# Kernel tuning notes

Hardware: AMD Instinct MI355X
Metric: run time of the kernel (lower is better)

## Reference

```python
import jax, jax.numpy as jnp
import numpy as np

E, H, V, B, T = 512, 512, 32000, 64, 20


def setup_inputs() -> dict:
    key = jax.random.key(0)
    ks = jax.random.split(key, 10)
    s = 0.05
    return {
        "features": jax.random.normal(ks[0], (B, E), jnp.float32),
        "captions": jax.random.randint(ks[1], (B, T), 0, V),
        "lenghts": jax.random.randint(ks[2], (B,), 1, T),
        "emb_table": jax.random.normal(ks[3], (V, E), jnp.float32) * s,
        "w_ih": jax.random.normal(ks[4], (4 * H, E), jnp.float32) * s,
        "w_hh": jax.random.normal(ks[5], (4 * H, H), jnp.float32) * s,
        "b_ih": jax.random.normal(ks[6], (4 * H,), jnp.float32) * s,
        "b_hh": jax.random.normal(ks[7], (4 * H,), jnp.float32) * s,
        "fc_w": jax.random.normal(ks[8], (V, H), jnp.float32) * s,
        "fc_b": jax.random.normal(ks[9], (V,), jnp.float32) * s,
    }


def _lstm(xs, w_ih, w_hh, b_ih, b_hh):
    # xs: [B, T+1, E] -> hidden states [B, T+1, H], PyTorch gate order i,f,g,o
    b, _, _ = xs.shape
    h0 = jnp.zeros((b, w_hh.shape[1]), xs.dtype)
    c0 = jnp.zeros_like(h0)
    bias = b_ih + b_hh

    def step(carry, x_t):
        h, c = carry
        gates = x_t @ w_ih.T + h @ w_hh.T + bias  # [B, 4H]
        i, f, g, o = jnp.split(gates, 4, axis=-1)
        i, f, o = jax.nn.sigmoid(i), jax.nn.sigmoid(f), jax.nn.sigmoid(o)
        g = jnp.tanh(g)
        c = f * c + i * g
        h = o * jnp.tanh(c)
        return (h, c), h

    _, hs = jax.lax.scan(step, (h0, c0), jnp.swapaxes(xs, 0, 1))  # hs: [T+1, B, H]
    return jnp.swapaxes(hs, 0, 1)


def reference(features, captions, lenghts, emb_table, w_ih, w_hh, b_ih, b_hh, fc_w, fc_b):
    embeddings = emb_table[captions]                       # [B, T, E]
    xs = jnp.concatenate([features[:, None, :], embeddings], axis=1)  # [B, T+1, E]
    hs = _lstm(xs, w_ih, w_hh, b_ih, b_hh)[:, 1:, :]       # [B, T, H]
    logits = hs @ fc_w.T + fc_b                            # [B, T, V]
    # original loops softmax over each 1-D vocab slice == softmax over last axis
    return jax.nn.softmax(logits, axis=-1)
```

## Files before the change

kernel.cpp:

```cpp
#include <hip/hip_runtime.h>
#include <cstdint>
#include <cstddef>

#define E_DIM 512
#define H_DIM 512
#define V_DIM 32000
#define B_DIM 64
#define T_DIM 20

typedef _Float16 f16;
typedef _Float16 f16x8 __attribute__((ext_vector_type(8)));
typedef _Float16 f16x4 __attribute__((ext_vector_type(4)));
typedef float    f32x4 __attribute__((ext_vector_type(4)));

__device__ __forceinline__ void async_lds16(void* lds, const void* g) {
  __builtin_amdgcn_global_load_lds(
      (const __attribute__((address_space(1))) uint32_t*)g,
      (__attribute__((address_space(3))) uint32_t*)lds, 16, 0, 0);
}

__device__ __forceinline__ float sigmoidf_(float x) {
  return 1.0f / (1.0f + expf(-x));
}

__global__ __launch_bounds__(128) void gather_x16_kernel(
    const float* __restrict__ features, const int* __restrict__ captions,
    const float* __restrict__ emb, f16* __restrict__ x16) {
  const int m = blockIdx.x;
  const int j = threadIdx.x;
  f16x4 r4 = {(f16)0.f, (f16)0.f, (f16)0.f, (f16)0.f};
  if (m < 1344) {
    const int b = m / 21;
    const int t = m % 21;
    const float* src = (t == 0)
        ? features + (size_t)b * E_DIM
        : emb + (size_t)captions[b * T_DIM + (t - 1)] * E_DIM;
    const float4 v = ((const float4*)src)[j];
    r4.x = (f16)v.x; r4.y = (f16)v.y; r4.z = (f16)v.z; r4.w = (f16)v.w;
  }
  ((f16x4*)(x16 + (size_t)m * 512))[j] = r4;
}

__global__ __launch_bounds__(256) void convert_w_kernel(
    const float* __restrict__ w, f16* __restrict__ w16) {
  const int i = blockIdx.x * 256 + threadIdx.x;
  const float4 v = ((const float4*)w)[i];
  f16x4 r;
  r.x = (f16)v.x; r.y = (f16)v.y; r.z = (f16)v.z; r.w = (f16)v.w;
  ((f16x4*)w16)[i] = r;
}

__global__ __launch_bounds__(256) void bias_sum_kernel(
    const float* __restrict__ a, const float* __restrict__ b,
    float* __restrict__ o) {
  const int i = blockIdx.x * 256 + threadIdx.x;
  if (i < 2048) o[i] = a[i] + b[i];
}

__global__ __launch_bounds__(256) void gemm16_kernel(
    const f16* __restrict__ A, const f16* __restrict__ Bw,
    const float* __restrict__ bias, float* __restrict__ C, int ldc) {
  __shared__ f16 As[128 * 64];
  __shared__ f16 Bs[128 * 64];
  const int tid = threadIdx.x;
  const int lane = tid & 63;
  const int wid = tid >> 6;
  const int m0 = blockIdx.y * 128;
  const int n0 = blockIdx.x * 128;
  const int wm = (wid >> 1) * 64;
  const int wn = (wid & 1) * 64;

  f32x4 acc[4][4];
#pragma unroll
  for (int i = 0; i < 4; ++i)
#pragma unroll
    for (int j = 0; j < 4; ++j) {
      f32x4 z = {0.f, 0.f, 0.f, 0.f};
      acc[i][j] = z;
    }
  const int lr = lane & 15;
  const int lkb = (lane >> 4) * 8;

  for (int kt = 0; kt < 512; kt += 64) {
#pragma unroll
    for (int i = 0; i < 4; ++i) {
      const int off = i * 4096 + wid * 1024 + lane * 16;
      const int row = off >> 7;
      const int colh = (off & 127) >> 1;
      async_lds16((char*)As + i * 4096 + wid * 1024,
                  A + (size_t)(m0 + row) * 512 + kt + colh);
      async_lds16((char*)Bs + i * 4096 + wid * 1024,
                  Bw + (size_t)(n0 + row) * 512 + kt + colh);
    }
    __syncthreads();
#pragma unroll
    for (int ks = 0; ks < 2; ++ks) {
      f16x8 af[4], bf[4];
#pragma unroll
      for (int mi = 0; mi < 4; ++mi)
        af[mi] = *(const f16x8*)&As[(wm + mi * 16 + lr) * 64 + ks * 32 + lkb];
#pragma unroll
      for (int ni = 0; ni < 4; ++ni)
        bf[ni] = *(const f16x8*)&Bs[(wn + ni * 16 + lr) * 64 + ks * 32 + lkb];
#pragma unroll
      for (int mi = 0; mi < 4; ++mi)
#pragma unroll
        for (int ni = 0; ni < 4; ++ni)
          acc[mi][ni] = __builtin_amdgcn_mfma_f32_16x16x32_f16(
              af[mi], bf[ni], acc[mi][ni], 0, 0, 0);
    }
    __syncthreads();
  }

#pragma unroll
  for (int mi = 0; mi < 4; ++mi) {
    const int mbase = m0 + wm + mi * 16 + (lane >> 4) * 4;
#pragma unroll
    for (int ni = 0; ni < 4; ++ni) {
      const int n = n0 + wn + ni * 16 + lr;
      const float bv = bias[n];
#pragma unroll
      for (int r = 0; r < 4; ++r)
        C[(size_t)(mbase + r) * ldc + n] = acc[mi][ni][r] + bv;
    }
  }
}

__global__ __launch_bounds__(256) void gemm16_f16out_kernel(
    const f16* __restrict__ A, const f16* __restrict__ Bw,
    const float* __restrict__ bias, f16* __restrict__ C16) {
  __shared__ f16 As[128 * 64];
  __shared__ f16 Bs[128 * 64];
  const int tid = threadIdx.x;
  const int lane = tid & 63;
  const int wid = tid >> 6;
  const int m0 = blockIdx.y * 128;
  const int n0 = blockIdx.x * 128;
  const int wm = (wid >> 1) * 64;
  const int wn = (wid & 1) * 64;

  f32x4 acc[4][4];
#pragma unroll
  for (int i = 0; i < 4; ++i)
#pragma unroll
    for (int j = 0; j < 4; ++j) {
      f32x4 z = {0.f, 0.f, 0.f, 0.f};
      acc[i][j] = z;
    }
  const int lr = lane & 15;
  const int lkb = (lane >> 4) * 8;

  for (int kt = 0; kt < 512; kt += 64) {
#pragma unroll
    for (int i = 0; i < 4; ++i) {
      const int off = i * 4096 + wid * 1024 + lane * 16;
      const int row = off >> 7;
      const int colh = (off & 127) >> 1;
      async_lds16((char*)As + i * 4096 + wid * 1024,
                  A + (size_t)(m0 + row) * 512 + kt + colh);
      async_lds16((char*)Bs + i * 4096 + wid * 1024,
                  Bw + (size_t)(n0 + row) * 512 + kt + colh);
    }
    __syncthreads();
#pragma unroll
    for (int ks = 0; ks < 2; ++ks) {
      f16x8 af[4], bf[4];
#pragma unroll
      for (int mi = 0; mi < 4; ++mi)
        af[mi] = *(const f16x8*)&As[(wm + mi * 16 + lr) * 64 + ks * 32 + lkb];
#pragma unroll
      for (int ni = 0; ni < 4; ++ni)
        bf[ni] = *(const f16x8*)&Bs[(wn + ni * 16 + lr) * 64 + ks * 32 + lkb];
#pragma unroll
      for (int mi = 0; mi < 4; ++mi)
#pragma unroll
        for (int ni = 0; ni < 4; ++ni)
          acc[mi][ni] = __builtin_amdgcn_mfma_f32_16x16x32_f16(
              af[mi], bf[ni], acc[mi][ni], 0, 0, 0);
    }
    __syncthreads();
  }

#pragma unroll
  for (int mi = 0; mi < 4; ++mi) {
    const int mbase = m0 + wm + mi * 16 + (lane >> 4) * 4;
#pragma unroll
    for (int ni = 0; ni < 4; ++ni) {
      const int n = n0 + wn + ni * 16 + lr;
      const float bv = bias[n];
#pragma unroll
      for (int r = 0; r < 4; ++r)
        C16[(size_t)(mbase + r) * 32000 + n] = (f16)(acc[mi][ni][r] + bv);
    }
  }
}

__global__ __launch_bounds__(256) void lstm_step_direct(
    const float* __restrict__ P, const f16* __restrict__ Whh,
    const f16* __restrict__ h_in, f16* __restrict__ h_out,
    float* __restrict__ c, f16* __restrict__ hs16, int t) {
  const int tid = threadIdx.x;
  const int lane = tid & 63;
  const int w = tid >> 6;
  const int u0 = blockIdx.x * 4;
  const int fr = lane & 15;
  const int fq = lane >> 4;
  const int grow = (fr >> 2) * 512 + u0 + (fr & 3);

  f32x4 acc = {0.f, 0.f, 0.f, 0.f};
  if (t > 0) {
    const f16* arow = h_in + (size_t)(w * 16 + fr) * 512;
    const f16* brow = Whh + (size_t)grow * 512;
    f16x8 a[16], b[16];
#pragma unroll
    for (int kk = 0; kk < 16; ++kk) {
      const int kc = kk * 32 + fq * 8;
      a[kk] = *(const f16x8*)&arow[kc];
      b[kk] = *(const f16x8*)&brow[kc];
    }
#pragma unroll
    for (int kk = 0; kk < 16; ++kk)
      acc = __builtin_amdgcn_mfma_f32_16x16x32_f16(a[kk], b[kk], acc, 0, 0, 0);
  }

#pragma unroll
  for (int r = 0; r < 4; ++r) {
    const int b = w * 16 + fq * 4 + r;
    acc[r] += P[((size_t)b * 21 + t) * 2048 + grow];
  }

#pragma unroll
  for (int r = 0; r < 4; ++r) {
    const float x  = acc[r];
    const float xf = __shfl_xor(x, 4);
    const float xg = __shfl_xor(x, 8);
    const float xo = __shfl_xor(x, 12);
    if (fr < 4) {
      const int b = w * 16 + fq * 4 + r;
      const int u = u0 + fr;
      const size_t bu = (size_t)b * 512 + u;
      const float si = sigmoidf_(x);
      const float sf = sigmoidf_(xf);
      const float tg = tanhf(xg);
      const float so = sigmoidf_(xo);
      const float cn = sf * c[bu] + si * tg;
      c[bu] = cn;
      const float hn = so * tanhf(cn);
      h_out[bu] = (f16)hn;
      if (t >= 1)
        hs16[((size_t)b * T_DIM + (t - 1)) * 512 + u] = (f16)hn;
    }
  }
}

__device__ __forceinline__ float waveMax(float v) {
#pragma unroll
  for (int o = 32; o > 0; o >>= 1) v = fmaxf(v, __shfl_down(v, o));
  return v;
}
__device__ __forceinline__ float waveSum(float v) {
#pragma unroll
  for (int o = 32; o > 0; o >>= 1) v += __shfl_down(v, o);
  return v;
}

__global__ __launch_bounds__(1024) void softmax_f16_kernel(
    const f16* __restrict__ lg, float* __restrict__ out) {
  const f16x8* L = (const f16x8*)(lg + (size_t)blockIdx.x * V_DIM);
  float4* p4 = (float4*)(out + (size_t)blockIdx.x * V_DIM);
  const int t = threadIdx.x;
  __shared__ float sred[16];

  float4 v[8];
  float m = -1e30f;
#pragma unroll
  for (int j = 0; j < 4; ++j) {
    const int i = j * 1024 + t;
    if (i < 4000) {
      const f16x8 h = L[i];
      v[2 * j].x     = (float)h[0]; v[2 * j].y     = (float)h[1];
      v[2 * j].z     = (float)h[2]; v[2 * j].w     = (float)h[3];
      v[2 * j + 1].x = (float)h[4]; v[2 * j + 1].y = (float)h[5];
      v[2 * j + 1].z = (float)h[6]; v[2 * j + 1].w = (float)h[7];
      m = fmaxf(m, fmaxf(fmaxf(v[2 * j].x, v[2 * j].y),
                         fmaxf(v[2 * j].z, v[2 * j].w)));
      m = fmaxf(m, fmaxf(fmaxf(v[2 * j + 1].x, v[2 * j + 1].y),
                         fmaxf(v[2 * j + 1].z, v[2 * j + 1].w)));
    }
  }
  m = waveMax(m);
  if ((t & 63) == 0) sred[t >> 6] = m;
  __syncthreads();
  float mb = sred[0];
#pragma unroll
  for (int k = 1; k < 16; ++k) mb = fmaxf(mb, sred[k]);
  __syncthreads();

  float s = 0.f;
#pragma unroll
  for (int j = 0; j < 8; ++j) {
    const int i = (j >> 1) * 1024 + t;
    if (i < 4000) {
      v[j].x = expf(v[j].x - mb);
      v[j].y = expf(v[j].y - mb);
      v[j].z = expf(v[j].z - mb);
      v[j].w = expf(v[j].w - mb);
      s += v[j].x + v[j].y + v[j].z + v[j].w;
    }
  }
  s = waveSum(s);
  if ((t & 63) == 0) sred[t >> 6] = s;
  __syncthreads();
  float sb = sred[0];
#pragma unroll
  for (int k = 1; k < 16; ++k) sb += sred[k];
  const float inv = 1.0f / sb;

#pragma unroll
  for (int j = 0; j < 4; ++j) {
    const int i = j * 1024 + t;
    if (i < 4000) {
      float4 a = v[2 * j], b = v[2 * j + 1];
      a.x *= inv; a.y *= inv; a.z *= inv; a.w *= inv;
      b.x *= inv; b.y *= inv; b.z *= inv; b.w *= inv;
      p4[2 * i] = a;
      p4[2 * i + 1] = b;
    }
  }
}

__global__ __launch_bounds__(1024) void softmax_reg_kernel(
    float* __restrict__ out) {
  float4* p4 = (float4*)(out + (size_t)blockIdx.x * V_DIM);
  const int t = threadIdx.x;
  __shared__ float sred[16];
  float4 v[8];
  float m = -1e30f;
#pragma unroll
  for (int j = 0; j < 8; ++j) {
    const int i = j * 1024 + t;
    if (i < 8000) {
      v[j] = p4[i];
      m = fmaxf(m, fmaxf(fmaxf(v[j].x, v[j].y), fmaxf(v[j].z, v[j].w)));
    }
  }
  m = waveMax(m);
  if ((t & 63) == 0) sred[t >> 6] = m;
  __syncthreads();
  float mb = sred[0];
#pragma unroll
  for (int k = 1; k < 16; ++k) mb = fmaxf(mb, sred[k]);
  __syncthreads();
  float s = 0.f;
#pragma unroll
  for (int j = 0; j < 8; ++j) {
    const int i = j * 1024 + t;
    if (i < 8000) {
      v[j].x = expf(v[j].x - mb);
      v[j].y = expf(v[j].y - mb);
      v[j].z = expf(v[j].z - mb);
      v[j].w = expf(v[j].w - mb);
      s += v[j].x + v[j].y + v[j].z + v[j].w;
    }
  }
  s = waveSum(s);
  if ((t & 63) == 0) sred[t >> 6] = s;
  __syncthreads();
  float sb = sred[0];
#pragma unroll
  for (int k = 1; k < 16; ++k) sb += sred[k];
  const float inv = 1.0f / sb;
#pragma unroll
  for (int j = 0; j < 8; ++j) {
    const int i = j * 1024 + t;
    if (i < 8000) {
      float4 o;
      o.x = v[j].x * inv; o.y = v[j].y * inv;
      o.z = v[j].z * inv; o.w = v[j].w * inv;
      p4[i] = o;
    }
  }
}

extern "C" void kernel_launch(void* const* d_in, const int* in_sizes, int n_in,
                              void* d_out, int out_size, void* d_ws, size_t ws_size,
                              hipStream_t stream) {
  const float* features = (const float*)d_in[0];
  const int*   captions = (const int*)d_in[1];
  const float* emb      = (const float*)d_in[3];
  const float* w_ih     = (const float*)d_in[4];
  const float* w_hh     = (const float*)d_in[5];
  const float* b_ih     = (const float*)d_in[6];
  const float* b_hh     = (const float*)d_in[7];
  const float* fc_w     = (const float*)d_in[8];
  const float* fc_b     = (const float*)d_in[9];
  float* out = (float*)d_out;

  char* ws = (char*)d_ws;
  float* c    = (float*)ws; ws += (size_t)B_DIM * H_DIM * 4;
  f16*   h16a = (f16*)ws;   ws += (size_t)B_DIM * H_DIM * 2;
  f16*   h16b = (f16*)ws;   ws += (size_t)B_DIM * H_DIM * 2;
  f16*   hs16 = (f16*)ws;   ws += (size_t)B_DIM * T_DIM * H_DIM * 2;
  f16*   w16  = (f16*)ws;   ws += (size_t)V_DIM * H_DIM * 2;
  f16*   logits16 = (f16*)ws;
  const size_t ws_need_f16logits =
      ((char*)logits16 - (char*)d_ws) + (size_t)1280 * V_DIM * 2;
  const bool use_f16_logits = ws_size >= ws_need_f16logits;

  float* P     = out;
  f16*   x16   = (f16*)(out + 3000000);
  f16*   wih16 = (f16*)(out + 3400000);
  f16*   whh16 = (f16*)(out + 4000000);
  float* bsum  = out + 4600000;

  hipMemsetAsync(c, 0, (size_t)B_DIM * H_DIM * 4, stream);

  gather_x16_kernel<<<1408, 128, 0, stream>>>(features, captions, emb, x16);
  convert_w_kernel<<<1024, 256, 0, stream>>>(w_ih, wih16);
  convert_w_kernel<<<1024, 256, 0, stream>>>(w_hh, whh16);
  convert_w_kernel<<<16000, 256, 0, stream>>>(fc_w, w16);
  bias_sum_kernel<<<8, 256, 0, stream>>>(b_ih, b_hh, bsum);

  gemm16_kernel<<<dim3(16, 11), 256, 0, stream>>>(x16, wih16, bsum, P, 2048);

  f16* hb[2] = {h16a, h16b};
  for (int t = 0; t <= T_DIM; ++t) {
    lstm_step_direct<<<128, 256, 0, stream>>>(P, whh16, hb[t & 1],
                                              hb[(t + 1) & 1], c, hs16, t);
  }

  if (use_f16_logits) {
    gemm16_f16out_kernel<<<dim3(250, 10), 256, 0, stream>>>(hs16, w16, fc_b,
                                                            logits16);
    softmax_f16_kernel<<<1280, 1024, 0, stream>>>(logits16, out);
  } else {
    gemm16_kernel<<<dim3(250, 10), 256, 0, stream>>>(hs16, w16, fc_b, out,
                                                     32000);
    softmax_reg_kernel<<<1280, 1024, 0, stream>>>(out);
  }
}
```

Measured before the change: 373.7 us.

## Replace per-timestep LSTM launches with persistent kernel using grid barrier

The 21 separate LSTM step launches are replaced by one persistent kernel of 128 blocks that loops over timesteps. Blocks synchronise through an atomic counter in global memory, with agent-scope atomic loads and stores for h, and the cell state stays in registers. The gathered input rows are reordered to time-major so each step's P rows are contiguous. This removes launch and inter-kernel gaps on the sequential recurrence, but it relies on all 128 blocks being co-resident and adds spin-barrier latency at each step.

```diff
diff --git a/kernel.cpp b/kernel.cpp
--- a/kernel.cpp
+++ b/kernel.cpp
@@ -7,6 +7,7 @@
 #define V_DIM 32000
 #define B_DIM 64
 #define T_DIM 20
+#define NBLK_LSTM 128
 
 typedef _Float16 f16;
 typedef _Float16 f16x8 __attribute__((ext_vector_type(8)));
@@ -21,6 +22,21 @@
 
 __device__ __forceinline__ float sigmoidf_(float x) {
   return 1.0f / (1.0f + expf(-x));
+}
+
+__device__ __forceinline__ f16x8 load_h8_coh(const f16* p) {
+  union { unsigned long long u[2]; f16x8 v; } r;
+  r.u[0] = __hip_atomic_load((const unsigned long long*)p,
+                             __ATOMIC_RELAXED, __HIP_MEMORY_SCOPE_AGENT);
+  r.u[1] = __hip_atomic_load((const unsigned long long*)(p + 4),
+                             __ATOMIC_RELAXED, __HIP_MEMORY_SCOPE_AGENT);
+  return r.v;
+}
+__device__ __forceinline__ void store_h_coh(f16* p, float v) {
+  union { f16 h; unsigned short s; } cvt;
+  cvt.h = (f16)v;
+  __hip_atomic_store((unsigned short*)p, cvt.s,
+                     __ATOMIC_RELAXED, __HIP_MEMORY_SCOPE_AGENT);
 }
 
 __global__ __launch_bounds__(128) void gather_x16_kernel(
@@ -30,8 +46,8 @@
   const int j = threadIdx.x;
   f16x4 r4 = {(f16)0.f, (f16)0.f, (f16)0.f, (f16)0.f};
   if (m < 1344) {
-    const int b = m / 21;
-    const int t = m % 21;
+    const int b = m & 63;
+    const int t = m >> 6;
     const float* src = (t == 0)
         ? features + (size_t)b * E_DIM
         : emb + (size_t)captions[b * T_DIM + (t - 1)] * E_DIM;
@@ -195,10 +211,10 @@
   }
 }
 
-__global__ __launch_bounds__(256) void lstm_step_direct(
+__global__ __launch_bounds__(256) void lstm_persistent2(
     const float* __restrict__ P, const f16* __restrict__ Whh,
-    const f16* __restrict__ h_in, f16* __restrict__ h_out,
-    float* __restrict__ c, f16* __restrict__ hs16, int t) {
+    f16* __restrict__ hA, f16* __restrict__ hB,
+    f16* __restrict__ hs16, unsigned* __restrict__ bar) {
   const int tid = threadIdx.x;
   const int lane = tid & 63;
   const int w = tid >> 6;
@@ -206,49 +222,68 @@
   const int fr = lane & 15;
   const int fq = lane >> 4;
   const int grow = (fr >> 2) * 512 + u0 + (fr & 3);
-
-  f32x4 acc = {0.f, 0.f, 0.f, 0.f};
-  if (t > 0) {
-    const f16* arow = h_in + (size_t)(w * 16 + fr) * 512;
-    const f16* brow = Whh + (size_t)grow * 512;
-    f16x8 a[16], b[16];
-#pragma unroll
-    for (int kk = 0; kk < 16; ++kk) {
-      const int kc = kk * 32 + fq * 8;
-      a[kk] = *(const f16x8*)&arow[kc];
-      b[kk] = *(const f16x8*)&brow[kc];
-    }
-#pragma unroll
-    for (int kk = 0; kk < 16; ++kk)
-      acc = __builtin_amdgcn_mfma_f32_16x16x32_f16(a[kk], b[kk], acc, 0, 0, 0);
-  }
-
-#pragma unroll
-  for (int r = 0; r < 4; ++r) {
-    const int b = w * 16 + fq * 4 + r;
-    acc[r] += P[((size_t)b * 21 + t) * 2048 + grow];
-  }
-
-#pragma unroll
-  for (int r = 0; r < 4; ++r) {
-    const float x  = acc[r];
-    const float xf = __shfl_xor(x, 4);
-    const float xg = __shfl_xor(x, 8);
-    const float xo = __shfl_xor(x, 12);
-    if (fr < 4) {
+  const f16* brow = Whh + (size_t)grow * 512;
+
+  float cr[4] = {0.f, 0.f, 0.f, 0.f};
+
+  for (int t = 0; t <= T_DIM; ++t) {
+    f32x4 acc = {0.f, 0.f, 0.f, 0.f};
+    if (t > 0) {
+      const f16* hin = (t & 1) ? hA : hB;
+      const f16* arow = hin + (size_t)(w * 16 + fr) * 512;
+      f16x8 a[16], b[16];
+#pragma unroll
+      for (int kk = 0; kk < 16; ++kk) {
+        const int kc = kk * 32 + fq * 8;
+        a[kk] = load_h8_coh(&arow[kc]);
+        b[kk] = *(const f16x8*)&brow[kc];
+      }
+#pragma unroll
+      for (int kk = 0; kk < 16; ++kk)
+        acc = __builtin_amdgcn_mfma_f32_16x16x32_f16(a[kk], b[kk], acc,
+                                                     0, 0, 0);
+    }
+#pragma unroll
+    for (int r = 0; r < 4; ++r) {
       const int b = w * 16 + fq * 4 + r;
-      const int u = u0 + fr;
-      const size_t bu = (size_t)b * 512 + u;
-      const float si = sigmoidf_(x);
-      const float sf = sigmoidf_(xf);
-      const float tg = tanhf(xg);
-      const float so = sigmoidf_(xo);
-      const float cn = sf * c[bu] + si * tg;
-      c[bu] = cn;
-      const float hn = so * tanhf(cn);
-      h_out[bu] = (f16)hn;
-      if (t >= 1)
-        hs16[((size_t)b * T_DIM + (t - 1)) * 512 + u] = (f16)hn;
+      acc[r] += P[((size_t)(t * 64 + b)) * 2048 + grow];
+    }
+
+    f16* hout = (t & 1) ? hB : hA;
+#pragma unroll
+    for (int r = 0; r < 4; ++r) {
+      const float x  = acc[r];
+      const float xf = __shfl_xor(x, 4);
+      const float xg = __shfl_xor(x, 8);
+      const float xo = __shfl_xor(x, 12);
+      if (fr < 4) {
+        const int b = w * 16 + fq * 4 + r;
+        const int u = u0 + fr;
+        const float si = sigmoidf_(x);
+        const float sf = sigmoidf_(xf);
+        const float tg = tanhf(xg);
+        const float so = sigmoidf_(xo);
+        const float cn = sf * cr[r] + si * tg;
+        cr[r] = cn;
+        const float hn = so * tanhf(cn);
+        store_h_coh(&hout[(size_t)b * 512 + u], hn);
+        if (t >= 1)
+          hs16[((size_t)b * T_DIM + (t - 1)) * 512 + u] = (f16)hn;
+      }
+    }
+
+    if (t < T_DIM) {
+      asm volatile("s_waitcnt vmcnt(0)" ::: "memory");
+      __syncthreads();
+      if (tid == 0) {
+        __hip_atomic_fetch_add(bar, 1u, __ATOMIC_RELAXED,
+                               __HIP_MEMORY_SCOPE_AGENT);
+        const unsigned target = (unsigned)(NBLK_LSTM * (t + 1));
+        while (__hip_atomic_load(bar, __ATOMIC_RELAXED,
+                                 __HIP_MEMORY_SCOPE_AGENT) < target)
+          __builtin_amdgcn_s_sleep(1);
+      }
+      __syncthreads();
     }
   }
 }
@@ -397,7 +432,7 @@
   float* out = (float*)d_out;
 
   char* ws = (char*)d_ws;
-  float* c    = (float*)ws; ws += (size_t)B_DIM * H_DIM * 4;
+  unsigned* bar = (unsigned*)ws; ws += 256;
   f16*   h16a = (f16*)ws;   ws += (size_t)B_DIM * H_DIM * 2;
   f16*   h16b = (f16*)ws;   ws += (size_t)B_DIM * H_DIM * 2;
   f16*   hs16 = (f16*)ws;   ws += (size_t)B_DIM * T_DIM * H_DIM * 2;
@@ -413,7 +448,7 @@
   f16*   whh16 = (f16*)(out + 4000000);
   float* bsum  = out + 4600000;
 
-  hipMemsetAsync(c, 0, (size_t)B_DIM * H_DIM * 4, stream);
+  hipMemsetAsync(bar, 0, 256, stream);
 
   gather_x16_kernel<<<1408, 128, 0, stream>>>(features, captions, emb, x16);
   convert_w_kernel<<<1024, 256, 0, stream>>>(w_ih, wih16);
@@ -423,11 +458,8 @@
 
   gemm16_kernel<<<dim3(16, 11), 256, 0, stream>>>(x16, wih16, bsum, P, 2048);
 
-  f16* hb[2] = {h16a, h16b};
-  for (int t = 0; t <= T_DIM; ++t) {
-    lstm_step_direct<<<128, 256, 0, stream>>>(P, whh16, hb[t & 1],
-                                              hb[(t + 1) & 1], c, hs16, t);
-  }
+  lstm_persistent2<<<NBLK_LSTM, 256, 0, stream>>>(P, whh16, h16a, h16b,
+                                                  hs16, bar);
 
   if (use_f16_logits) {
     gemm16_f16out_kernel<<<dim3(250, 10), 256, 0, stream>>>(hs16, w16, fc_b,
```

Measured after the change: 426.5 us. +14.1%, slower.
